# Kernel optimization log

Measured on AMD Instinct MI355X. Metric: run time of the kernel, lower is better.

The kernel has to match this reference:

```python
import jax, jax.numpy as jnp
import numpy as np

HIDDEN = 1024
HEADS = 16
HEAD_DIM = HIDDEN // HEADS

def setup_inputs() -> dict:
    key = jax.random.key(0)
    k1, k2, k3 = jax.random.split(key, 3)
    scale = 1.0 / np.sqrt(HIDDEN)
    return {
        "x": jax.random.normal(k1, (2, 2048, HIDDEN), dtype=jnp.float32),
        "w_qkv": jax.random.normal(k2, (HIDDEN, 3 * HIDDEN), dtype=jnp.float32) * scale,
        "b_qkv": jnp.zeros((3 * HIDDEN,), dtype=jnp.float32),
        "w_out": jax.random.normal(k3, (HIDDEN, HIDDEN), dtype=jnp.float32) * scale,
        "b_out": jnp.zeros((HIDDEN,), dtype=jnp.float32),
    }

def reference(x, w_qkv, b_qkv, w_out, b_out):
    B, S, H = x.shape
    qkv = x @ w_qkv + b_qkv                              # (B,S,3H)
    qkv = qkv.reshape(B, S, 3, HEADS, HEAD_DIM)
    qkv = jnp.transpose(qkv, (2, 0, 3, 1, 4))            # (3,B,nh,S,hd)
    q, k, v = qkv[0], qkv[1], qkv[2]
    scores = jnp.einsum("bhqd,bhkd->bhqk", q, k) / np.sqrt(HEAD_DIM)
    causal = jnp.triu(jnp.ones((S, S), dtype=bool), k=1)  # True above diagonal
    scores = jnp.where(causal, -jnp.inf, scores)
    attn = jax.nn.softmax(scores, axis=-1)               # dropout: eval mode (identity)
    out = jnp.einsum("bhqk,bhkd->bhqd", attn, v)
    out = jnp.transpose(out, (0, 2, 1, 3)).reshape(B, S, H)
    return out @ w_out + b_out
```

## Files before the change

kernel.cpp:

```cpp
#include <hip/hip_runtime.h>
#include <hip/hip_bf16.h>

typedef short short8 __attribute__((ext_vector_type(8)));
typedef float f32x4 __attribute__((ext_vector_type(4)));

typedef const __attribute__((address_space(1))) unsigned int* gas_ptr;
typedef __attribute__((address_space(3))) unsigned int* las_ptr;
#define ASYNC16(g, l) __builtin_amdgcn_global_load_lds((gas_ptr)(g), (las_ptr)(l), 16, 0, 0)

__device__ __forceinline__ unsigned short f2bf(float f) {
    unsigned int u = __builtin_bit_cast(unsigned int, f);
    u += 0x7fff + ((u >> 16) & 1);
    return (unsigned short)(u >> 16);
}
__device__ __forceinline__ float bf2f(unsigned short s) {
    unsigned int u = (unsigned int)s << 16;
    return __builtin_bit_cast(float, u);
}
__device__ __forceinline__ unsigned int pkbf_trunc(float lo, float hi) {
    return __builtin_amdgcn_perm(__builtin_bit_cast(unsigned int, hi),
                                 __builtin_bit_cast(unsigned int, lo), 0x07060302u);
}

__global__ __launch_bounds__(256) void cast_f32_bf16(
    const float* __restrict__ in, unsigned short* __restrict__ out, int n)
{
    int i = (blockIdx.x * 256 + threadIdx.x) * 4;
    if (i >= n) return;
    float4 v = *(const float4*)(in + i);
    ushort4 o;
    o.x = f2bf(v.x); o.y = f2bf(v.y); o.z = f2bf(v.z); o.w = f2bf(v.w);
    *(ushort4*)(out + i) = o;
}

__global__ __launch_bounds__(256) void transpose_cast(
    const float* __restrict__ w, unsigned short* __restrict__ wt, int K, int N)
{
    __shared__ unsigned short tile[64 * 65];
    int k0 = blockIdx.y * 64, n0 = blockIdx.x * 64;
    for (int i = threadIdx.x; i < 64 * 64; i += 256) {
        int r = i >> 6, c = i & 63;
        tile[r * 65 + c] = f2bf(w[(size_t)(k0 + r) * N + n0 + c]);
    }
    __syncthreads();
    for (int i = threadIdx.x; i < 64 * 64; i += 256) {
        int r = i >> 6, c = i & 63;
        wt[(size_t)(n0 + r) * K + k0 + c] = tile[c * 65 + r];
    }
}


template<bool OUT_BF16, bool QKV>
__global__ __launch_bounds__(256, 3) void gemm_bt(
    const unsigned short* __restrict__ A,
    const unsigned short* __restrict__ Bt,
    const float* __restrict__ bias,
    void* __restrict__ C,
    unsigned short* __restrict__ vTp,
    int M, int N, int K)
{
    __shared__ __align__(16) unsigned short As[128 * 32];
    __shared__ __align__(16) unsigned short Bs[128 * 32];
    const int tid = threadIdx.x;
    const int lane = tid & 63;
    const int wave = tid >> 6;
    const int wr = wave >> 1, wc = wave & 1;
    const int m0 = blockIdx.x * 128, n0 = blockIdx.y * 128;
    const int fr = lane & 15, fq = lane >> 4;

    f32x4 acc[4][4] = {};

    const int grow = lane >> 2;
    const int gcol = (lane & 3) * 8;
    const unsigned short* Ag = A  + (size_t)(m0 + wave * 32 + grow) * K + gcol;
    const unsigned short* Bg = Bt + (size_t)(n0 + wave * 32 + grow) * K + gcol;
    unsigned short* AsW0 = As + (wave * 32) * 32;
    unsigned short* AsW1 = As + (wave * 32 + 16) * 32;
    unsigned short* BsW0 = Bs + (wave * 32) * 32;
    unsigned short* BsW1 = Bs + (wave * 32 + 16) * 32;

    for (int k0 = 0; k0 < K; k0 += 32) {
        __syncthreads();
        ASYNC16(Ag + k0,          AsW0);
        ASYNC16(Ag + 16 * K + k0, AsW1);
        ASYNC16(Bg + k0,          BsW0);
        ASYNC16(Bg + 16 * K + k0, BsW1);
        __syncthreads();

        short8 af[4], bfr[4];
#pragma unroll
        for (int i = 0; i < 4; i++)
            af[i] = *(const short8*)(As + (wr * 64 + i * 16 + fr) * 32 + fq * 8);
#pragma unroll
        for (int j = 0; j < 4; j++)
            bfr[j] = *(const short8*)(Bs + (wc * 64 + j * 16 + fr) * 32 + fq * 8);
#pragma unroll
        for (int i = 0; i < 4; i++)
#pragma unroll
            for (int j = 0; j < 4; j++)
                acc[i][j] = __builtin_amdgcn_mfma_f32_16x16x32_bf16(af[i], bfr[j], acc[i][j], 0, 0, 0);
    }

#pragma unroll
    for (int i = 0; i < 4; i++)
#pragma unroll
        for (int j = 0; j < 4; j++) {
            int col = n0 + wc * 64 + j * 16 + fr;
            float bv = bias[col];
            if (QKV && col >= 2048) {
                int hh = (col - 2048) >> 6, d = col & 63;
#pragma unroll
                for (int r = 0; r < 4; r++) {
                    int row = m0 + wr * 64 + i * 16 + fq * 4 + r;
                    int bb = row >> 11, s = row & 2047;
                    vTp[((size_t)(bb * 16 + hh) * 64 + d) * 2048 + s] = f2bf(acc[i][j][r] + bv);
                }
            } else {
                const int cstride = QKV ? 2048 : N;
#pragma unroll
                for (int r = 0; r < 4; r++) {
                    int row = m0 + wr * 64 + i * 16 + fq * 4 + r;
                    float v = acc[i][j][r] + bv;
                    if (OUT_BF16)
                        ((unsigned short*)C)[(size_t)row * cstride + col] = f2bf(v);
                    else
                        ((float*)C)[(size_t)row * cstride + col] = v;
                }
            }
        }
}


template<int RG0>
__device__ __forceinline__ void attn_step(
    const unsigned short* __restrict__ Ks0, const unsigned short* __restrict__ Ks1,
    const unsigned short* __restrict__ Vs0, const unsigned short* __restrict__ Vs1,
    unsigned short* __restrict__ Psw,
    const short8 (&qf)[2][2], const short8 ones,
    f32x4 (&o_acc)[2][4], f32x4 (&l_acc)[2],
    int j0, int fr, int fq,
    const int (&qrow0)[2], const bool (&diag)[2])
{
    f32x4 s[2][4];
#pragma unroll
    for (int rg = RG0; rg < 2; rg++)
#pragma unroll
        for (int t = 0; t < 4; t++)
            s[rg][t] = (f32x4){0.f, 0.f, 0.f, 0.f};

#pragma unroll
    for (int t = 0; t < 4; t++) {
        short8 kf0 = *(const short8*)(Ks0 + (t * 16 + fr) * 32 + fq * 8);
        short8 kf1 = *(const short8*)(Ks1 + (t * 16 + fr) * 32 + fq * 8);
#pragma unroll
        for (int rg = RG0; rg < 2; rg++) {
            s[rg][t] = __builtin_amdgcn_mfma_f32_16x16x32_bf16(qf[rg][0], kf0, s[rg][t], 0, 0, 0);
            s[rg][t] = __builtin_amdgcn_mfma_f32_16x16x32_bf16(qf[rg][1], kf1, s[rg][t], 0, 0, 0);
        }
    }

#pragma unroll
    for (int rg = RG0; rg < 2; rg++) {
        unsigned short* prow = Psw + rg * (16 * 64);
#pragma unroll
        for (int t = 0; t < 4; t++) {
            float p[4];
#pragma unroll
            for (int r = 0; r < 4; r++) {
                float v = __expf(s[rg][t][r] * 0.125f - 8.0f);
                if (diag[rg] && (j0 + t * 16 + fr) > (qrow0[rg] + fq * 4 + r)) v = 0.f;
                p[r] = v;
            }
            unsigned int pk01 = pkbf_trunc(p[0], p[1]);
            unsigned int pk23 = pkbf_trunc(p[2], p[3]);
            int colp = (t * 16 + fr + 16 * fq) & 63;
            int base = (fq * 4) * 64 + colp;
            prow[base]       = (unsigned short)pk01;
            prow[base + 64]  = (unsigned short)(pk01 >> 16);
            prow[base + 128] = (unsigned short)pk23;
            prow[base + 192] = (unsigned short)(pk23 >> 16);
        }
    }

#pragma unroll
    for (int ks = 0; ks < 2; ks++) {
        const unsigned short* Vsb = ks ? Vs1 : Vs0;
        short8 pf[2];
#pragma unroll
        for (int rg = RG0; rg < 2; rg++) {
            int colp = (ks * 32 + fq * 8 + 16 * ((fr >> 2) & 3)) & 63;
            pf[rg] = *(const short8*)(Psw + rg * (16 * 64) + fr * 64 + colp);
        }
#pragma unroll
        for (int t = 0; t < 4; t++) {
            short8 vf = *(const short8*)(Vsb + (t * 16 + fr) * 32 + fq * 8);
#pragma unroll
            for (int rg = RG0; rg < 2; rg++)
                o_acc[rg][t] = __builtin_amdgcn_mfma_f32_16x16x32_bf16(pf[rg], vf, o_acc[rg][t], 0, 0, 0);
        }
#pragma unroll
        for (int rg = RG0; rg < 2; rg++)
            l_acc[rg] = __builtin_amdgcn_mfma_f32_16x16x32_bf16(pf[rg], ones, l_acc[rg], 0, 0, 0);
    }
}

__global__ __launch_bounds__(256, 4) void flash_attn(
    const unsigned short* __restrict__ qkv,
    const unsigned short* __restrict__ vT,
    unsigned short* __restrict__ Opart,
    float* __restrict__ lpart)
{
    const int p = blockIdx.x;
    const int g = blockIdx.y;
    const int h = blockIdx.z & 15, b = blockIdx.z >> 4;
    const int qtA = p, qtB = 31 - p;
    const int tid = threadIdx.x, wave = tid >> 6, lane = tid & 63;
    const int fr = lane & 15, fq = lane >> 4;
    const size_t RS = 2048;

    const unsigned short* Qb = qkv + (size_t)b * 2048 * RS + h * 64;
    const unsigned short* Kb = Qb + 1024;
    const unsigned short* Vt = vT + (size_t)(b * 16 + h) * 64 * 2048;

    __shared__ __align__(16) unsigned short Ks[2][64 * 32];
    __shared__ __align__(16) unsigned short Vs[2][64 * 32];
    __shared__ __align__(16) unsigned short Ps[4][2 * 16 * 64];

    short8 qf[2][2];
    int qrow0[2];
#pragma unroll
    for (int rg = 0; rg < 2; rg++) {
        int qt = rg ? qtB : qtA;
        qrow0[rg] = qt * 64 + wave * 16;
        const unsigned short* qrow = Qb + (size_t)(qrow0[rg] + fr) * RS;
        qf[rg][0] = *(const short8*)(qrow + fq * 8);
        qf[rg][1] = *(const short8*)(qrow + 32 + fq * 8);
    }
    short8 ones;
#pragma unroll
    for (int e = 0; e < 8; e++) ones[e] = (short)0x3F80;

    f32x4 o_acc[2][4] = {};
    f32x4 l_acc[2] = {};

    const int grow = lane >> 2;
    const int gcol = (lane & 3) * 8;
    const unsigned short* Kg = Kb + (size_t)(wave * 16 + grow) * RS + gcol;
    const unsigned short* Vg = Vt + (size_t)(wave * 16 + grow) * 2048 + gcol;
    unsigned short* KsW0 = Ks[0] + (wave * 16) * 32;
    unsigned short* KsW1 = Ks[1] + (wave * 16) * 32;
    unsigned short* VsW0 = Vs[0] + (wave * 16) * 32;
    unsigned short* VsW1 = Vs[1] + (wave * 16) * 32;

    const int mid = (p >= 8) ? 8 : (16 - p);
    const int lo = g ? mid : 0;
    const int hi = g ? (32 - p) : mid;

    for (int jt = lo; jt < hi; jt++) {
        const int j0 = jt * 64;
        __syncthreads();
        ASYNC16(Kg + (size_t)j0 * RS,      KsW0);
        ASYNC16(Kg + (size_t)j0 * RS + 32, KsW1);
        ASYNC16(Vg + j0,      VsW0);
        ASYNC16(Vg + j0 + 32, VsW1);
        __syncthreads();

        bool diag[2] = { jt == qtA, jt == qtB };
        if (jt <= qtA)
            attn_step<0>(Ks[0], Ks[1], Vs[0], Vs[1], Ps[wave], qf, ones,
                         o_acc, l_acc, j0, fr, fq, qrow0, diag);
        else
            attn_step<1>(Ks[0], Ks[1], Vs[0], Vs[1], Ps[wave], qf, ones,
                         o_acc, l_acc, j0, fr, fq, qrow0, diag);
    }

    unsigned short* Og = Opart + (size_t)g * 4096 * 1024;
    float* lg = lpart + (size_t)g * 4096 * 16;
#pragma unroll
    for (int rg = 0; rg < 2; rg++) {
#pragma unroll
        for (int t = 0; t < 4; t++)
#pragma unroll
            for (int r = 0; r < 4; r++) {
                int row = qrow0[rg] + fq * 4 + r;
                Og[(size_t)(b * 2048 + row) * 1024 + h * 64 + t * 16 + fr] = f2bf(o_acc[rg][t][r]);
            }
        if (fr == 0) {
#pragma unroll
            for (int r = 0; r < 4; r++) {
                int row = qrow0[rg] + fq * 4 + r;
                lg[(size_t)(b * 2048 + row) * 16 + h] = l_acc[rg][r];
            }
        }
    }
}

__global__ __launch_bounds__(256) void reduce_attn(
    const unsigned short* __restrict__ Opart, const float* __restrict__ lpart,
    unsigned short* __restrict__ out)
{
    int i = (blockIdx.x * 256 + threadIdx.x) * 8;
    int row = i >> 10, h = (i & 1023) >> 6;
    float lsum = lpart[(size_t)row * 16 + h] + lpart[(size_t)4096 * 16 + row * 16 + h];
    float inv = 1.0f / lsum;
    ushort4 a0 = *(const ushort4*)(Opart + i);
    ushort4 a1 = *(const ushort4*)(Opart + i + 4);
    ushort4 b0 = *(const ushort4*)(Opart + (size_t)4096 * 1024 + i);
    ushort4 b1 = *(const ushort4*)(Opart + (size_t)4096 * 1024 + i + 4);
    ushort4 o0, o1;
    o0.x = f2bf((bf2f(a0.x) + bf2f(b0.x)) * inv);
    o0.y = f2bf((bf2f(a0.y) + bf2f(b0.y)) * inv);
    o0.z = f2bf((bf2f(a0.z) + bf2f(b0.z)) * inv);
    o0.w = f2bf((bf2f(a0.w) + bf2f(b0.w)) * inv);
    o1.x = f2bf((bf2f(a1.x) + bf2f(b1.x)) * inv);
    o1.y = f2bf((bf2f(a1.y) + bf2f(b1.y)) * inv);
    o1.z = f2bf((bf2f(a1.z) + bf2f(b1.z)) * inv);
    o1.w = f2bf((bf2f(a1.w) + bf2f(b1.w)) * inv);
    *(ushort4*)(out + i) = o0;
    *(ushort4*)(out + i + 4) = o1;
}

extern "C" void kernel_launch(void* const* d_in, const int* in_sizes, int n_in,
                              void* d_out, int out_size, void* d_ws, size_t ws_size,
                              hipStream_t stream) {
    const float* x      = (const float*)d_in[0];
    const float* w_qkv  = (const float*)d_in[1];
    const float* b_qkv  = (const float*)d_in[2];
    const float* w_out  = (const float*)d_in[3];
    const float* b_out  = (const float*)d_in[4];
    float* out = (float*)d_out;

    char* ws = (char*)d_ws;
    unsigned short* x_b    = (unsigned short*)(ws);
    unsigned short* wqkv_t = (unsigned short*)(ws + 8u  * 1024 * 1024);
    unsigned short* wout_t = (unsigned short*)(ws + 14u * 1024 * 1024);
    unsigned short* qkv    = (unsigned short*)(ws + 16u * 1024 * 1024);
    unsigned short* attn   = (unsigned short*)(ws + 32u * 1024 * 1024);
    unsigned short* vT     = (unsigned short*)(ws + 40u * 1024 * 1024);
    unsigned short* Opart  = (unsigned short*)(ws + 48u * 1024 * 1024);
    float*          lpart  = (float*)         (ws + 64u * 1024 * 1024);

    cast_f32_bf16<<<4096, 256, 0, stream>>>(x, x_b, 2 * 2048 * 1024);
    transpose_cast<<<dim3(48, 16), 256, 0, stream>>>(w_qkv, wqkv_t, 1024, 3072);
    transpose_cast<<<dim3(16, 16), 256, 0, stream>>>(w_out, wout_t, 1024, 1024);
    gemm_bt<true, true ><<<dim3(32, 24), 256, 0, stream>>>(x_b,  wqkv_t, b_qkv, qkv, vT, 4096, 3072, 1024);
    flash_attn<<<dim3(16, 2, 32), 256, 0, stream>>>(qkv, vT, Opart, lpart);
    reduce_attn<<<2048, 256, 0, stream>>>(Opart, lpart, attn);
    gemm_bt<false, false><<<dim3(32, 8),  256, 0, stream>>>(attn, wout_t, b_out, out, nullptr, 4096, 1024, 1024);
}
```

Before: 206.9 us.

## Merge prep kernels and give each attention wave 32 query rows

The cast and two weight-transpose kernels become a single launch, which removes two kernel launches. The attention kernel now runs 128 threads per block, and each of its two waves handles four 16-row query groups instead of two, so every K fragment loaded from LDS is reused across more rows. The causal mask check is also split into a diagonal and a non-diagonal path, so most tiles skip the per-element compare. The cost is more registers per wave (twice the accumulators and query fragments) and fewer waves per block, which can lower occupancy and latency hiding.

```diff
diff --git a/kernel.cpp b/kernel.cpp
--- a/kernel.cpp
+++ b/kernel.cpp
@@ -22,22 +22,10 @@
                                  __builtin_bit_cast(unsigned int, lo), 0x07060302u);
 }
 
-__global__ __launch_bounds__(256) void cast_f32_bf16(
-    const float* __restrict__ in, unsigned short* __restrict__ out, int n)
-{
-    int i = (blockIdx.x * 256 + threadIdx.x) * 4;
-    if (i >= n) return;
-    float4 v = *(const float4*)(in + i);
-    ushort4 o;
-    o.x = f2bf(v.x); o.y = f2bf(v.y); o.z = f2bf(v.z); o.w = f2bf(v.w);
-    *(ushort4*)(out + i) = o;
-}
-
-__global__ __launch_bounds__(256) void transpose_cast(
-    const float* __restrict__ w, unsigned short* __restrict__ wt, int K, int N)
-{
-    __shared__ unsigned short tile[64 * 65];
-    int k0 = blockIdx.y * 64, n0 = blockIdx.x * 64;
+__device__ __forceinline__ void transpose_tile(
+    const float* __restrict__ w, unsigned short* __restrict__ wt,
+    int K, int N, int k0, int n0, unsigned short* tile)
+{
     for (int i = threadIdx.x; i < 64 * 64; i += 256) {
         int r = i >> 6, c = i & 63;
         tile[r * 65 + c] = f2bf(w[(size_t)(k0 + r) * N + n0 + c]);
@@ -46,6 +34,29 @@
     for (int i = threadIdx.x; i < 64 * 64; i += 256) {
         int r = i >> 6, c = i & 63;
         wt[(size_t)(n0 + r) * K + k0 + c] = tile[c * 65 + r];
+    }
+}
+
+__global__ __launch_bounds__(256) void prep(
+    const float* __restrict__ x, const float* __restrict__ w_qkv,
+    const float* __restrict__ w_out,
+    unsigned short* __restrict__ x_b, unsigned short* __restrict__ wqkv_t,
+    unsigned short* __restrict__ wout_t)
+{
+    __shared__ unsigned short tile[64 * 65];
+    int bid = blockIdx.x;
+    if (bid < 4096) {
+        int i = (bid * 256 + threadIdx.x) * 4;
+        float4 v = *(const float4*)(x + i);
+        ushort4 o;
+        o.x = f2bf(v.x); o.y = f2bf(v.y); o.z = f2bf(v.z); o.w = f2bf(v.w);
+        *(ushort4*)(x_b + i) = o;
+    } else if (bid < 4096 + 768) {
+        int t = bid - 4096;
+        transpose_tile(w_qkv, wqkv_t, 1024, 3072, (t / 48) * 64, (t % 48) * 64, tile);
+    } else {
+        int t = bid - 4864;
+        transpose_tile(w_out, wout_t, 1024, 1024, (t >> 4) * 64, (t & 15) * 64, tile);
     }
 }
 
@@ -136,75 +147,87 @@
     const unsigned short* __restrict__ Ks0, const unsigned short* __restrict__ Ks1,
     const unsigned short* __restrict__ Vs0, const unsigned short* __restrict__ Vs1,
     unsigned short* __restrict__ Psw,
-    const short8 (&qf)[2][2], const short8 ones,
-    f32x4 (&o_acc)[2][4], f32x4 (&l_acc)[2],
+    const short8 (&qf)[4][2], const short8 ones,
+    f32x4 (&o_acc)[4][4], f32x4 (&l_acc)[4],
     int j0, int fr, int fq,
-    const int (&qrow0)[2], const bool (&diag)[2])
-{
-    f32x4 s[2][4];
-#pragma unroll
-    for (int rg = RG0; rg < 2; rg++)
-#pragma unroll
-        for (int t = 0; t < 4; t++)
-            s[rg][t] = (f32x4){0.f, 0.f, 0.f, 0.f};
-
+    const int (&qrow0)[4], bool diagA, bool diagB)
+{
+    short8 kf[4][2];
 #pragma unroll
     for (int t = 0; t < 4; t++) {
-        short8 kf0 = *(const short8*)(Ks0 + (t * 16 + fr) * 32 + fq * 8);
-        short8 kf1 = *(const short8*)(Ks1 + (t * 16 + fr) * 32 + fq * 8);
-#pragma unroll
-        for (int rg = RG0; rg < 2; rg++) {
-            s[rg][t] = __builtin_amdgcn_mfma_f32_16x16x32_bf16(qf[rg][0], kf0, s[rg][t], 0, 0, 0);
-            s[rg][t] = __builtin_amdgcn_mfma_f32_16x16x32_bf16(qf[rg][1], kf1, s[rg][t], 0, 0, 0);
-        }
-    }
-
-#pragma unroll
-    for (int rg = RG0; rg < 2; rg++) {
+        kf[t][0] = *(const short8*)(Ks0 + (t * 16 + fr) * 32 + fq * 8);
+        kf[t][1] = *(const short8*)(Ks1 + (t * 16 + fr) * 32 + fq * 8);
+    }
+
+#pragma unroll
+    for (int rg = RG0; rg < 4; rg++) {
+        f32x4 s[4];
+#pragma unroll
+        for (int t = 0; t < 4; t++) {
+            s[t] = (f32x4){0.f, 0.f, 0.f, 0.f};
+            s[t] = __builtin_amdgcn_mfma_f32_16x16x32_bf16(qf[rg][0], kf[t][0], s[t], 0, 0, 0);
+            s[t] = __builtin_amdgcn_mfma_f32_16x16x32_bf16(qf[rg][1], kf[t][1], s[t], 0, 0, 0);
+        }
+        const bool diag = (rg < 2) ? diagA : diagB;
         unsigned short* prow = Psw + rg * (16 * 64);
-#pragma unroll
-        for (int t = 0; t < 4; t++) {
-            float p[4];
-#pragma unroll
-            for (int r = 0; r < 4; r++) {
-                float v = __expf(s[rg][t][r] * 0.125f - 8.0f);
-                if (diag[rg] && (j0 + t * 16 + fr) > (qrow0[rg] + fq * 4 + r)) v = 0.f;
-                p[r] = v;
-            }
-            unsigned int pk01 = pkbf_trunc(p[0], p[1]);
-            unsigned int pk23 = pkbf_trunc(p[2], p[3]);
-            int colp = (t * 16 + fr + 16 * fq) & 63;
-            int base = (fq * 4) * 64 + colp;
-            prow[base]       = (unsigned short)pk01;
-            prow[base + 64]  = (unsigned short)(pk01 >> 16);
-            prow[base + 128] = (unsigned short)pk23;
-            prow[base + 192] = (unsigned short)(pk23 >> 16);
+        if (diag) {
+#pragma unroll
+            for (int t = 0; t < 4; t++) {
+                float p[4];
+#pragma unroll
+                for (int r = 0; r < 4; r++) {
+                    float v = __expf(s[t][r] * 0.125f - 8.0f);
+                    if ((j0 + t * 16 + fr) > (qrow0[rg] + fq * 4 + r)) v = 0.f;
+                    p[r] = v;
+                }
+                unsigned int pk01 = pkbf_trunc(p[0], p[1]);
+                unsigned int pk23 = pkbf_trunc(p[2], p[3]);
+                int base = (fq * 4) * 64 + ((t * 16 + fr + 16 * fq) & 63);
+                prow[base]       = (unsigned short)pk01;
+                prow[base + 64]  = (unsigned short)(pk01 >> 16);
+                prow[base + 128] = (unsigned short)pk23;
+                prow[base + 192] = (unsigned short)(pk23 >> 16);
+            }
+        } else {
+#pragma unroll
+            for (int t = 0; t < 4; t++) {
+                float p[4];
+#pragma unroll
+                for (int r = 0; r < 4; r++)
+                    p[r] = __expf(s[t][r] * 0.125f - 8.0f);
+                unsigned int pk01 = pkbf_trunc(p[0], p[1]);
+                unsigned int pk23 = pkbf_trunc(p[2], p[3]);
+                int base = (fq * 4) * 64 + ((t * 16 + fr + 16 * fq) & 63);
+                prow[base]       = (unsigned short)pk01;
+                prow[base + 64]  = (unsigned short)(pk01 >> 16);
+                prow[base + 128] = (unsigned short)pk23;
+                prow[base + 192] = (unsigned short)(pk23 >> 16);
+            }
         }
     }
 
 #pragma unroll
     for (int ks = 0; ks < 2; ks++) {
         const unsigned short* Vsb = ks ? Vs1 : Vs0;
-        short8 pf[2];
-#pragma unroll
-        for (int rg = RG0; rg < 2; rg++) {
-            int colp = (ks * 32 + fq * 8 + 16 * ((fr >> 2) & 3)) & 63;
+        const int colp = (ks * 32 + fq * 8 + 16 * ((fr >> 2) & 3)) & 63;
+        short8 pf[4];
+#pragma unroll
+        for (int rg = RG0; rg < 4; rg++)
             pf[rg] = *(const short8*)(Psw + rg * (16 * 64) + fr * 64 + colp);
-        }
 #pragma unroll
         for (int t = 0; t < 4; t++) {
             short8 vf = *(const short8*)(Vsb + (t * 16 + fr) * 32 + fq * 8);
 #pragma unroll
-            for (int rg = RG0; rg < 2; rg++)
+            for (int rg = RG0; rg < 4; rg++)
                 o_acc[rg][t] = __builtin_amdgcn_mfma_f32_16x16x32_bf16(pf[rg], vf, o_acc[rg][t], 0, 0, 0);
         }
 #pragma unroll
-        for (int rg = RG0; rg < 2; rg++)
+        for (int rg = RG0; rg < 4; rg++)
             l_acc[rg] = __builtin_amdgcn_mfma_f32_16x16x32_bf16(pf[rg], ones, l_acc[rg], 0, 0, 0);
     }
 }
 
-__global__ __launch_bounds__(256, 4) void flash_attn(
+__global__ __launch_bounds__(128, 2) void flash_attn(
     const unsigned short* __restrict__ qkv,
     const unsigned short* __restrict__ vT,
     unsigned short* __restrict__ Opart,
@@ -213,7 +236,6 @@
     const int p = blockIdx.x;
     const int g = blockIdx.y;
     const int h = blockIdx.z & 15, b = blockIdx.z >> 4;
-    const int qtA = p, qtB = 31 - p;
     const int tid = threadIdx.x, wave = tid >> 6, lane = tid & 63;
     const int fr = lane & 15, fq = lane >> 4;
     const size_t RS = 2048;
@@ -224,14 +246,14 @@
 
     __shared__ __align__(16) unsigned short Ks[2][64 * 32];
     __shared__ __align__(16) unsigned short Vs[2][64 * 32];
-    __shared__ __align__(16) unsigned short Ps[4][2 * 16 * 64];
-
-    short8 qf[2][2];
-    int qrow0[2];
-#pragma unroll
-    for (int rg = 0; rg < 2; rg++) {
-        int qt = rg ? qtB : qtA;
-        qrow0[rg] = qt * 64 + wave * 16;
+    __shared__ __align__(16) unsigned short Ps[2][4 * 16 * 64];
+
+    short8 qf[4][2];
+    int qrow0[4];
+#pragma unroll
+    for (int rg = 0; rg < 4; rg++) {
+        int qt = (rg < 2) ? p : (31 - p);
+        qrow0[rg] = qt * 64 + wave * 32 + (rg & 1) * 16;
         const unsigned short* qrow = Qb + (size_t)(qrow0[rg] + fr) * RS;
         qf[rg][0] = *(const short8*)(qrow + fq * 8);
         qf[rg][1] = *(const short8*)(qrow + 32 + fq * 8);
@@ -240,17 +262,21 @@
 #pragma unroll
     for (int e = 0; e < 8; e++) ones[e] = (short)0x3F80;
 
-    f32x4 o_acc[2][4] = {};
-    f32x4 l_acc[2] = {};
+    f32x4 o_acc[4][4] = {};
+    f32x4 l_acc[4] = {};
 
     const int grow = lane >> 2;
     const int gcol = (lane & 3) * 8;
-    const unsigned short* Kg = Kb + (size_t)(wave * 16 + grow) * RS + gcol;
-    const unsigned short* Vg = Vt + (size_t)(wave * 16 + grow) * 2048 + gcol;
-    unsigned short* KsW0 = Ks[0] + (wave * 16) * 32;
-    unsigned short* KsW1 = Ks[1] + (wave * 16) * 32;
-    unsigned short* VsW0 = Vs[0] + (wave * 16) * 32;
-    unsigned short* VsW1 = Vs[1] + (wave * 16) * 32;
+    const unsigned short* Kg = Kb + (size_t)(wave * 32 + grow) * RS + gcol;
+    const unsigned short* Vg = Vt + (size_t)(wave * 32 + grow) * 2048 + gcol;
+    unsigned short* KsW00 = Ks[0] + (wave * 32) * 32;
+    unsigned short* KsW01 = Ks[0] + (wave * 32 + 16) * 32;
+    unsigned short* KsW10 = Ks[1] + (wave * 32) * 32;
+    unsigned short* KsW11 = Ks[1] + (wave * 32 + 16) * 32;
+    unsigned short* VsW00 = Vs[0] + (wave * 32) * 32;
+    unsigned short* VsW01 = Vs[0] + (wave * 32 + 16) * 32;
+    unsigned short* VsW10 = Vs[1] + (wave * 32) * 32;
+    unsigned short* VsW11 = Vs[1] + (wave * 32 + 16) * 32;
 
     const int mid = (p >= 8) ? 8 : (16 - p);
     const int lo = g ? mid : 0;
@@ -259,25 +285,29 @@
     for (int jt = lo; jt < hi; jt++) {
         const int j0 = jt * 64;
         __syncthreads();
-        ASYNC16(Kg + (size_t)j0 * RS,      KsW0);
-        ASYNC16(Kg + (size_t)j0 * RS + 32, KsW1);
-        ASYNC16(Vg + j0,      VsW0);
-        ASYNC16(Vg + j0 + 32, VsW1);
+        ASYNC16(Kg + (size_t)j0 * RS,               KsW00);
+        ASYNC16(Kg + (size_t)(j0 + 16) * RS,        KsW01);
+        ASYNC16(Kg + (size_t)j0 * RS + 32,          KsW10);
+        ASYNC16(Kg + (size_t)(j0 + 16) * RS + 32,   KsW11);
+        ASYNC16(Vg + j0,               VsW00);
+        ASYNC16(Vg + 16 * 2048 + j0,   VsW01);
+        ASYNC16(Vg + j0 + 32,          VsW10);
+        ASYNC16(Vg + 16 * 2048 + j0 + 32, VsW11);
         __syncthreads();
 
-        bool diag[2] = { jt == qtA, jt == qtB };
-        if (jt <= qtA)
+        bool diagA = (jt == p), diagB = (jt == 31 - p);
+        if (jt <= p)
             attn_step<0>(Ks[0], Ks[1], Vs[0], Vs[1], Ps[wave], qf, ones,
-                         o_acc, l_acc, j0, fr, fq, qrow0, diag);
+                         o_acc, l_acc, j0, fr, fq, qrow0, diagA, diagB);
         else
-            attn_step<1>(Ks[0], Ks[1], Vs[0], Vs[1], Ps[wave], qf, ones,
-                         o_acc, l_acc, j0, fr, fq, qrow0, diag);
+            attn_step<2>(Ks[0], Ks[1], Vs[0], Vs[1], Ps[wave], qf, ones,
+                         o_acc, l_acc, j0, fr, fq, qrow0, diagA, diagB);
     }
 
     unsigned short* Og = Opart + (size_t)g * 4096 * 1024;
     float* lg = lpart + (size_t)g * 4096 * 16;
 #pragma unroll
-    for (int rg = 0; rg < 2; rg++) {
+    for (int rg = 0; rg < 4; rg++) {
 #pragma unroll
         for (int t = 0; t < 4; t++)
 #pragma unroll
@@ -340,11 +370,9 @@
     unsigned short* Opart  = (unsigned short*)(ws + 48u * 1024 * 1024);
     float*          lpart  = (float*)         (ws + 64u * 1024 * 1024);
 
-    cast_f32_bf16<<<4096, 256, 0, stream>>>(x, x_b, 2 * 2048 * 1024);
-    transpose_cast<<<dim3(48, 16), 256, 0, stream>>>(w_qkv, wqkv_t, 1024, 3072);
-    transpose_cast<<<dim3(16, 16), 256, 0, stream>>>(w_out, wout_t, 1024, 1024);
+    prep<<<5120, 256, 0, stream>>>(x, w_qkv, w_out, x_b, wqkv_t, wout_t);
     gemm_bt<true, true ><<<dim3(32, 24), 256, 0, stream>>>(x_b,  wqkv_t, b_qkv, qkv, vT, 4096, 3072, 1024);
-    flash_attn<<<dim3(16, 2, 32), 256, 0, stream>>>(qkv, vT, Opart, lpart);
+    flash_attn<<<dim3(16, 2, 32), 128, 0, stream>>>(qkv, vT, Opart, lpart);
     reduce_attn<<<2048, 256, 0, stream>>>(Opart, lpart, attn);
     gemm_bt<false, false><<<dim3(32, 8),  256, 0, stream>>>(attn, wout_t, b_out, out, nullptr, 4096, 1024, 1024);
 }
```

After: 193.0 us. 1.07x faster.
